# Performance work log

Hardware: AMD Instinct MI355X
Metric: run time of the kernel (lower is better)

The kernel has to match this reference:

```python
import jax, jax.numpy as jnp
import numpy as np

EPS = 1e-12  # torch F.normalize default eps


def setup_inputs() -> dict:
    key = jax.random.key(0)
    ks = jax.random.split(key, 7)
    dim, heads = 128, 8
    b, c, s, h, w = 2, dim, 3, 128, 128
    sc = 1.0 / np.sqrt(dim)
    return {
        "x": jax.random.normal(ks[0], (b, c, s, h, w), dtype=jnp.float32),
        "Wq": jax.random.normal(ks[1], (dim, dim), dtype=jnp.float32) * sc,
        "Wk": jax.random.normal(ks[2], (dim, dim), dtype=jnp.float32) * sc,
        "Wv": jax.random.normal(ks[3], (dim, dim), dtype=jnp.float32) * sc,
        "Wp": jax.random.normal(ks[4], (dim, dim), dtype=jnp.float32) * sc,
        "bp": jax.random.normal(ks[5], (dim,), dtype=jnp.float32) * 0.01,
        "rescale": jnp.ones((heads, 1, 1), dtype=jnp.float32),
    }


def _l2norm(t):
    # torch F.normalize(p=2, dim=-1): t / max(||t||, eps)
    n = jnp.sqrt(jnp.sum(t * t, axis=-1, keepdims=True))
    return t / jnp.maximum(n, EPS)


def reference(x, Wq, Wk, Wv, Wp, bp, rescale):
    b, c, s, h, w = x.shape
    heads = rescale.shape[0]
    d = c // heads
    n = h * w * s
    # [b,c,s,h,w] -> [b,h,w,s,c] -> [b, n, c]
    xt = jnp.transpose(x, (0, 3, 4, 2, 1)).reshape(b, n, c)
    # torch Linear: y = x @ W.T
    q = xt @ Wq.T
    k = xt @ Wk.T
    v = xt @ Wv.T
    # [b,n,heads,d] -> [b,heads,d,n] (channel attention: tokens along last axis)
    def to_heads(t):
        return jnp.transpose(t.reshape(b, n, heads, d), (0, 2, 3, 1))
    q, k, v = to_heads(q), to_heads(k), to_heads(v)
    q = _l2norm(q)
    k = _l2norm(k)
    # attn: [b,heads,d,d] = k @ q^T over token axis n
    attn = jnp.einsum('bhdn,bhen->bhde', k, q)
    attn = attn * rescale  # rescale broadcasts as [heads,1,1]
    attn = jax.nn.softmax(attn, axis=-1)
    out = jnp.einsum('bhde,bhen->bhdn', attn, v)  # [b,heads,d,n]
    # [b,heads,d,n] -> [b,n,heads*d]
    out = jnp.transpose(out, (0, 3, 1, 2)).reshape(b, n, c)
    out = out @ Wp.T + bp
    # [b,n,c] -> [b,h,w,s,c] -> [b,h,w,c,s] -> [b,c,s,h,w]
    out = out.reshape(b, h, w, s, c)
    out = jnp.transpose(out, (0, 1, 2, 4, 3))
    out = jnp.transpose(out, (0, 3, 4, 1, 2))
    return out
```

## Files before the change

kernel.cpp:

```cpp
#include <hip/hip_runtime.h>
#include <hip/hip_bf16.h>

typedef __bf16 bf16_t;
typedef __bf16 bf16x4 __attribute__((ext_vector_type(4)));
typedef __bf16 bf16x8 __attribute__((ext_vector_type(8)));
typedef float f32x4 __attribute__((ext_vector_type(4)));

#define NTOK 49152
#define CDIM 128
#define CHUNKS 128
#define KT 384
#define STEPS 12

__device__ inline f32x4 mfma16(bf16x8 a, bf16x8 b, f32x4 c) {
  return __builtin_amdgcn_mfma_f32_16x16x32_bf16(a, b, c, 0, 0, 0);
}

#define BARRIER() do { asm volatile("s_waitcnt lgkmcnt(0)" ::: "memory"); \
    __builtin_amdgcn_s_barrier(); } while (0)

__global__ __launch_bounds__(256) void k1_gram(const float* __restrict__ x,
                                               float* __restrict__ part) {
  const int blk = blockIdx.x;
  const int b = blk >> 7, chunk = blk & 127;
  const float* Xb = x + (size_t)b * CDIM * NTOK;
  const int tid = threadIdx.x, wave = tid >> 6, lane = tid & 63;

  __shared__ __align__(16) bf16_t tile[2][128 * 32];

  const int sch = tid >> 1, shalf = tid & 1;
  const float* gsrc = Xb + (size_t)sch * NTOK + chunk * KT + shalf * 16;
  const int c16base = ((sch >> 4) << 6) + (sch & 15);
  const int cg0 = c16base + ((shalf * 2) << 4);
  const int cg1 = c16base + ((shalf * 2 + 1) << 4);

  f32x4 stA[4], stB[4];
#define STAGE_LOAD(st, step)                               \
  {                                                        \
    const float* p_ = gsrc + (step) * 32;                  \
    st[0] = *(const f32x4*)(p_ + 0);                       \
    st[1] = *(const f32x4*)(p_ + 4);                       \
    st[2] = *(const f32x4*)(p_ + 8);                       \
    st[3] = *(const f32x4*)(p_ + 12);                      \
  }
#define CVT4(v) (bf16x4){(bf16_t)(v)[0], (bf16_t)(v)[1], (bf16_t)(v)[2], (bf16_t)(v)[3]}
#define STAGE_WRITE(st, buf)                               \
  {                                                        \
    bf16_t* t_ = &tile[buf][0];                            \
    *(bf16x4*)&t_[cg0 * 8 + 0] = CVT4(st[0]);              \
    *(bf16x4*)&t_[cg0 * 8 + 4] = CVT4(st[1]);              \
    *(bf16x4*)&t_[cg1 * 8 + 0] = CVT4(st[2]);              \
    *(bf16x4*)&t_[cg1 * 8 + 4] = CVT4(st[3]);              \
  }

  f32x4 acc[2][8];
#pragma unroll
  for (int t = 0; t < 2; ++t)
#pragma unroll
    for (int j = 0; j < 8; ++j) acc[t][j] = (f32x4){0.f, 0.f, 0.f, 0.f};

#define MFMA_PHASE(buf)                                                     \
  {                                                                         \
    bf16x8 frag[8];                                                         \
    _Pragma("unroll")                                                       \
    for (int g = 0; g < 8; ++g)                                             \
      frag[g] = *(const bf16x8*)&tile[buf][(g * 64 + lane) * 8];            \
    bf16x8 a0, a1;                                                          \
    if (wave == 0)      { a0 = frag[0]; a1 = frag[1]; }                     \
    else if (wave == 1) { a0 = frag[2]; a1 = frag[3]; }                     \
    else if (wave == 2) { a0 = frag[4]; a1 = frag[5]; }                     \
    else                { a0 = frag[6]; a1 = frag[7]; }                     \
    _Pragma("unroll")                                                       \
    for (int j = 0; j < 8; ++j) {                                           \
      acc[0][j] = mfma16(a0, frag[j], acc[0][j]);                           \
      acc[1][j] = mfma16(a1, frag[j], acc[1][j]);                           \
    }                                                                       \
  }

  STAGE_LOAD(stA, 0);
  STAGE_WRITE(stA, 0);
  STAGE_LOAD(stB, 1);
  BARRIER();

  for (int kk = 0; kk < STEPS; kk += 2) {
    if (kk + 2 < STEPS) STAGE_LOAD(stA, kk + 2);
    STAGE_WRITE(stB, 1);
    MFMA_PHASE(0);
    BARRIER();
    if (kk + 3 < STEPS) STAGE_LOAD(stB, kk + 3);
    if (kk + 2 < STEPS) STAGE_WRITE(stA, 0);
    MFMA_PHASE(1);
    BARRIER();
  }
#undef STAGE_LOAD
#undef STAGE_WRITE
#undef MFMA_PHASE

  float* pb = part + ((size_t)(b * CHUNKS + chunk) << 14);
#pragma unroll
  for (int t = 0; t < 2; ++t)
#pragma unroll
    for (int j = 0; j < 8; ++j)
      *(f32x4*)&pb[((((t * 8 + j) << 8) + tid) << 2)] = acc[t][j];
}

__global__ __launch_bounds__(256) void k2a_reduce(const float* __restrict__ part,
                                                  float* __restrict__ part2) {
  const int gid = blockIdx.x * 256 + threadIdx.x;
  const int e4 = gid & 4095, sl = (gid >> 12) & 7, b = gid >> 15;
  const float* p = part + ((size_t)(b * CHUNKS + sl * 16) << 14) + e4 * 4;
  f32x4 s = (f32x4){0.f, 0.f, 0.f, 0.f};
#pragma unroll 8
  for (int i = 0; i < 16; ++i) s += *(const f32x4*)(p + ((size_t)i << 14));
  *(f32x4*)(part2 + ((size_t)(b * 8 + sl) << 14) + e4 * 4) = s;
}

__global__ __launch_bounds__(256) void k2b_reduce(const float* __restrict__ part2,
                                                  float* __restrict__ S) {
  const int gid = blockIdx.x * 256 + threadIdx.x;
  const int g4 = gid & 4095, b = gid >> 12;
  f32x4 s = (f32x4){0.f, 0.f, 0.f, 0.f};
#pragma unroll
  for (int sl = 0; sl < 8; ++sl)
    s += *(const f32x4*)(part2 + ((size_t)(b * 8 + sl) << 14) + g4 * 4);
  const int tj = g4 >> 8, t = tj >> 3, j = tj & 7;
  const int tid2 = g4 & 255, wave = tid2 >> 6, quad = (tid2 >> 4) & 3, r = tid2 & 15;
  const int row0 = wave * 32 + t * 16 + quad * 4, col = j * 16 + r;
  float* Sb = S + ((size_t)b << 14);
#pragma unroll
  for (int reg = 0; reg < 4; ++reg) Sb[(row0 + reg) * 128 + col] = s[reg];
}

__global__ __launch_bounds__(256) void k3_t(const float* __restrict__ S,
                                            const float* __restrict__ Wk,
                                            const float* __restrict__ Wq,
                                            float* __restrict__ Tm) {
  const int idx = blockIdx.x * 256 + threadIdx.x;
  const int j = idx & 127, i = (idx >> 7) & 127, t = (idx >> 14) & 1, b = idx >> 15;
  const f32x4* w4 = (const f32x4*)((t ? Wq : Wk) + i * 128);
  const f32x4* s4 = (const f32x4*)(S + (b << 14) + j * 128);
  float s = 0.f;
#pragma unroll 8
  for (int q = 0; q < 32; ++q) {
    const f32x4 a = w4[q], v = s4[q];
    s += a[0] * v[0] + a[1] * v[1] + a[2] * v[2] + a[3] * v[3];
  }
  Tm[idx] = s;
}

__global__ __launch_bounds__(256) void k3_attn(const float* __restrict__ Tm,
                                               const float* __restrict__ Wk,
                                               const float* __restrict__ Wq,
                                               const float* __restrict__ resc,
                                               float* __restrict__ attn) {
  const int blk = blockIdx.x;
  const int b = blk >> 3, h = blk & 7;
  const int tid = threadIdx.x, d = tid >> 4, e = tid & 15;
  const float* Tk = Tm + (size_t)(b * 2 + 0) * 16384;
  const float* Tq = Tm + (size_t)(b * 2 + 1) * 16384;

  const float* tkrow = Tk + (h * 16 + d) * 128;
  const float* wqrow = Wq + (h * 16 + e) * 128;
  float g = 0.f;
#pragma unroll 4
  for (int c = 0; c < 128; ++c) g += tkrow[c] * wqrow[c];

  __shared__ float sqk[16], sqq[16];
  if (e == 0) {
    const float* wkrow = Wk + (h * 16 + d) * 128;
    float s = 0.f;
    for (int c = 0; c < 128; ++c) s += tkrow[c] * wkrow[c];
    sqk[d] = s;
  }
  if (d == 0) {
    const float* tqrow = Tq + (h * 16 + e) * 128;
    float s = 0.f;
    for (int c = 0; c < 128; ++c) s += tqrow[c] * wqrow[c];
    sqq[e] = s;
  }
  __syncthreads();

  const float nk = fmaxf(sqrtf(fmaxf(sqk[d], 0.f)), 1e-12f);
  const float nq = fmaxf(sqrtf(fmaxf(sqq[e], 0.f)), 1e-12f);
  float pre = g / (nk * nq) * resc[h];

  float mx = pre;
#pragma unroll
  for (int m = 1; m < 16; m <<= 1) mx = fmaxf(mx, __shfl_xor(mx, m, 64));
  const float p = expf(pre - mx);
  float sum = p;
#pragma unroll
  for (int m = 1; m < 16; m <<= 1) sum += __shfl_xor(sum, m, 64);
  attn[blk * 256 + tid] = p / sum;
}

__global__ __launch_bounds__(256) void k3_p(const float* __restrict__ attn,
                                            const float* __restrict__ Wp,
                                            const float* __restrict__ Wv,
                                            bf16_t* __restrict__ Phi) {
  const int blk = blockIdx.x;
  const int b = blk >> 7, rrow = blk & 127;
  const int tid = threadIdx.x;
  __shared__ float M[128];
  if (tid < 128) {
    const int h = tid >> 4, e = tid & 15;
    const float* A = attn + (size_t)(b * 8 + h) * 256;
    const float* wp = Wp + rrow * 128 + h * 16;
    float m = 0.f;
#pragma unroll
    for (int d = 0; d < 16; ++d) m += wp[d] * A[d * 16 + e];
    M[tid] = m;
  }
  __syncthreads();
  if (tid < 128) {
    const int c = tid;
    float p = 0.f;
#pragma unroll 4
    for (int j = 0; j < 128; ++j) p += M[j] * Wv[j * 128 + c];
    Phi[((size_t)b << 14) + rrow * 128 + c] = (bf16_t)p;
  }
}

__global__ __launch_bounds__(256) void k4_out(const float* __restrict__ x,
                                              const bf16_t* __restrict__ Phi,
                                              const float* __restrict__ bp,
                                              float* __restrict__ out) {
  const int blk = blockIdx.x;
  const int b = blk / 768, tg = blk % 768;
  const float* Xb = x + (size_t)b * CDIM * NTOK;
  const bf16_t* Ph = Phi + ((size_t)b << 14);
  float* Ob = out + (size_t)b * CDIM * NTOK;
  const int tid = threadIdx.x, wave = tid >> 6, lane = tid & 63;
  const int r = lane & 15, quad = lane >> 4;
  const int tok0 = tg * 64;

  __shared__ __align__(16) char smem[64 * 68 * 4];
  bf16_t* tile = (bf16_t*)smem;
  float* tbuf = (float*)smem;

  {
    const int sch = tid >> 1, shalf = tid & 1;
    const float* p = Xb + (size_t)sch * NTOK + tok0 + shalf * 32;
    f32x4 st[8];
#pragma unroll
    for (int q = 0; q < 8; ++q) st[q] = *(const f32x4*)(p + q * 4);
    const int chunk_hi = ((sch >> 5) << 8) + (((sch >> 3) & 3) << 4);
    const int ei = sch & 7;
#pragma unroll
    for (int j = 0; j < 32; ++j) {
      const int tok = shalf * 32 + j;
      const int chunk = chunk_hi + ((tok >> 4) << 6) + (tok & 15);
      tile[chunk * 8 + ei] = (bf16_t)st[j >> 2][j & 3];
    }
  }
  __syncthreads();

  f32x4 acc[8];
#pragma unroll
  for (int m = 0; m < 8; ++m) acc[m] = (f32x4){0.f, 0.f, 0.f, 0.f};

#pragma unroll
  for (int step = 0; step < 4; ++step) {
    const bf16x8 bfr = *(const bf16x8*)&tile[(step * 256 + wave * 64 + lane) * 8];
#pragma unroll
    for (int m = 0; m < 8; ++m) {
      const bf16x8 ah = *(const bf16x8*)(Ph + (16 * m + r) * 128 + step * 32 + quad * 8);
      acc[m] = mfma16(ah, bfr, acc[m]);
    }
  }

  __syncthreads();
#pragma unroll
  for (int half = 0; half < 2; ++half) {
#pragma unroll
    for (int mm = 0; mm < 4; ++mm) {
#pragma unroll
      for (int reg = 0; reg < 4; ++reg)
        tbuf[(mm * 16 + quad * 4 + reg) * 68 + wave * 16 + r] = acc[half * 4 + mm][reg];
    }
    __syncthreads();
#pragma unroll
    for (int rep = 0; rep < 4; ++rep) {
      const int idx = rep * 256 + tid, rloc = idx >> 4, g = idx & 15;
      f32x4 v = *(const f32x4*)&tbuf[rloc * 68 + g * 4];
      const int row = half * 64 + rloc;
      const float bb = bp[row];
      v[0] += bb; v[1] += bb; v[2] += bb; v[3] += bb;
      *(f32x4*)&Ob[(size_t)row * NTOK + tok0 + g * 4] = v;
    }
    if (half == 0) __syncthreads();
  }
}

extern "C" void kernel_launch(void* const* d_in, const int* in_sizes, int n_in,
                              void* d_out, int out_size, void* d_ws, size_t ws_size,
                              hipStream_t stream) {
  const float* x    = (const float*)d_in[0];
  const float* Wq   = (const float*)d_in[1];
  const float* Wk   = (const float*)d_in[2];
  const float* Wv   = (const float*)d_in[3];
  const float* Wp   = (const float*)d_in[4];
  const float* bp   = (const float*)d_in[5];
  const float* resc = (const float*)d_in[6];
  float* out = (float*)d_out;

  char* ws = (char*)d_ws;
  float*  S    = (float*)(ws + 0);
  float*  Tm   = (float*)(ws + 131072);
  float*  attn = (float*)(ws + 393216);
  bf16_t* Phi  = (bf16_t*)(ws + 409600);
  float* part  = (float*)d_out;
  float* part2 = (float*)((char*)d_out + 16777216);

  k1_gram<<<2 * CHUNKS, 256, 0, stream>>>(x, part);
  k2a_reduce<<<256, 256, 0, stream>>>(part, part2);
  k2b_reduce<<<32, 256, 0, stream>>>(part2, S);
  k3_t<<<256, 256, 0, stream>>>(S, Wk, Wq, Tm);
  k3_attn<<<16, 256, 0, stream>>>(Tm, Wk, Wq, resc, attn);
  k3_p<<<256, 256, 0, stream>>>(attn, Wp, Wv, Phi);
  k4_out<<<1536, 256, 0, stream>>>(x, Phi, bp, out);
}
```

Baseline: 180.0 us.

## Fuse all seven stages into one cooperative kernel with grid syncs

```diff
diff --git a/kernel.cpp b/kernel.cpp
--- a/kernel.cpp
+++ b/kernel.cpp
@@ -1,5 +1,8 @@
 #include <hip/hip_runtime.h>
 #include <hip/hip_bf16.h>
+#include <hip/hip_cooperative_groups.h>
+
+namespace cg = cooperative_groups;
 
 typedef __bf16 bf16_t;
 typedef __bf16 bf16x4 __attribute__((ext_vector_type(4)));
@@ -19,22 +22,6 @@
 #define BARRIER() do { asm volatile("s_waitcnt lgkmcnt(0)" ::: "memory"); \
     __builtin_amdgcn_s_barrier(); } while (0)
 
-__global__ __launch_bounds__(256) void k1_gram(const float* __restrict__ x,
-                                               float* __restrict__ part) {
-  const int blk = blockIdx.x;
-  const int b = blk >> 7, chunk = blk & 127;
-  const float* Xb = x + (size_t)b * CDIM * NTOK;
-  const int tid = threadIdx.x, wave = tid >> 6, lane = tid & 63;
-
-  __shared__ __align__(16) bf16_t tile[2][128 * 32];
-
-  const int sch = tid >> 1, shalf = tid & 1;
-  const float* gsrc = Xb + (size_t)sch * NTOK + chunk * KT + shalf * 16;
-  const int c16base = ((sch >> 4) << 6) + (sch & 15);
-  const int cg0 = c16base + ((shalf * 2) << 4);
-  const int cg1 = c16base + ((shalf * 2 + 1) << 4);
-
-  f32x4 stA[4], stB[4];
 #define STAGE_LOAD(st, step)                               \
   {                                                        \
     const float* p_ = gsrc + (step) * 32;                  \
@@ -52,13 +39,6 @@
     *(bf16x4*)&t_[cg1 * 8 + 0] = CVT4(st[2]);              \
     *(bf16x4*)&t_[cg1 * 8 + 4] = CVT4(st[3]);              \
   }
-
-  f32x4 acc[2][8];
-#pragma unroll
-  for (int t = 0; t < 2; ++t)
-#pragma unroll
-    for (int j = 0; j < 8; ++j) acc[t][j] = (f32x4){0.f, 0.f, 0.f, 0.f};
-
 #define MFMA_PHASE(buf)                                                     \
   {                                                                         \
     bf16x8 frag[8];                                                         \
@@ -77,6 +57,259 @@
     }                                                                       \
   }
 
+__global__ __launch_bounds__(256) void fused_all(
+    const float* x, const float* Wq, const float* Wk, const float* Wv,
+    const float* Wp, const float* bp, const float* resc,
+    float* S, float* Tm, float* attn, bf16_t* Phi, float* out) {
+  cg::grid_group grid = cg::this_grid();
+  const int blk = blockIdx.x;
+  const int tid = threadIdx.x, wave = tid >> 6, lane = tid & 63;
+  const int r = lane & 15, quad = lane >> 4;
+  float* part  = out;
+  float* part2 = out + (16777216 / 4);
+
+  __shared__ __align__(16) char smem[64 * 68 * 4];
+
+  {
+    bf16_t (*tile)[128 * 32] = (bf16_t (*)[128 * 32])smem;
+    const int b = blk >> 7, chunk = blk & 127;
+    const float* Xb = x + (size_t)b * CDIM * NTOK;
+    const int sch = tid >> 1, shalf = tid & 1;
+    const float* gsrc = Xb + (size_t)sch * NTOK + chunk * KT + shalf * 16;
+    const int c16base = ((sch >> 4) << 6) + (sch & 15);
+    const int cg0 = c16base + ((shalf * 2) << 4);
+    const int cg1 = c16base + ((shalf * 2 + 1) << 4);
+
+    f32x4 stA[4], stB[4];
+    f32x4 acc[2][8];
+#pragma unroll
+    for (int t = 0; t < 2; ++t)
+#pragma unroll
+      for (int j = 0; j < 8; ++j) acc[t][j] = (f32x4){0.f, 0.f, 0.f, 0.f};
+
+    STAGE_LOAD(stA, 0);
+    STAGE_WRITE(stA, 0);
+    STAGE_LOAD(stB, 1);
+    BARRIER();
+
+    for (int kk = 0; kk < STEPS; kk += 2) {
+      if (kk + 2 < STEPS) STAGE_LOAD(stA, kk + 2);
+      STAGE_WRITE(stB, 1);
+      MFMA_PHASE(0);
+      BARRIER();
+      if (kk + 3 < STEPS) STAGE_LOAD(stB, kk + 3);
+      if (kk + 2 < STEPS) STAGE_WRITE(stA, 0);
+      MFMA_PHASE(1);
+      BARRIER();
+    }
+
+    float* pb = part + ((size_t)(b * CHUNKS + chunk) << 14);
+#pragma unroll
+    for (int t = 0; t < 2; ++t)
+#pragma unroll
+      for (int j = 0; j < 8; ++j)
+        *(f32x4*)&pb[((((t * 8 + j) << 8) + tid) << 2)] = acc[t][j];
+  }
+  grid.sync();
+
+  {
+    const int gid = blk * 256 + tid;
+    const int e4 = gid & 4095, sl = (gid >> 12) & 7, b = gid >> 15;
+    const float* p = part + ((size_t)(b * CHUNKS + sl * 16) << 14) + e4 * 4;
+    f32x4 s0 = (f32x4){0.f, 0.f, 0.f, 0.f}, s1 = (f32x4){0.f, 0.f, 0.f, 0.f};
+#pragma unroll 4
+    for (int i = 0; i < 16; i += 2) {
+      s0 += *(const f32x4*)(p + ((size_t)i << 14));
+      s1 += *(const f32x4*)(p + ((size_t)(i + 1) << 14));
+    }
+    f32x4 s = s0 + s1;
+    *(f32x4*)(part2 + ((size_t)(b * 8 + sl) << 14) + e4 * 4) = s;
+  }
+  grid.sync();
+
+  if (blk < 32) {
+    const int gid = blk * 256 + tid;
+    const int g4 = gid & 4095, b = gid >> 12;
+    f32x4 s = (f32x4){0.f, 0.f, 0.f, 0.f};
+#pragma unroll
+    for (int sl = 0; sl < 8; ++sl)
+      s += *(const f32x4*)(part2 + ((size_t)(b * 8 + sl) << 14) + g4 * 4);
+    const int tj = g4 >> 8, t = tj >> 3, j = tj & 7;
+    const int tid2 = g4 & 255, w2 = tid2 >> 6, q2 = (tid2 >> 4) & 3, r2 = tid2 & 15;
+    const int row0 = w2 * 32 + t * 16 + q2 * 4, col = j * 16 + r2;
+    float* Sb = S + ((size_t)b << 14);
+#pragma unroll
+    for (int reg = 0; reg < 4; ++reg) Sb[(row0 + reg) * 128 + col] = s[reg];
+  }
+  grid.sync();
+
+  {
+    const int idx = blk * 256 + tid;
+    const int j = idx & 127, i = (idx >> 7) & 127, t = (idx >> 14) & 1, b = idx >> 15;
+    const f32x4* w4 = (const f32x4*)((t ? Wq : Wk) + i * 128);
+    const f32x4* s4 = (const f32x4*)(S + (b << 14) + j * 128);
+    float s = 0.f;
+#pragma unroll 8
+    for (int q = 0; q < 32; ++q) {
+      const f32x4 a = w4[q], v = s4[q];
+      s += a[0] * v[0] + a[1] * v[1] + a[2] * v[2] + a[3] * v[3];
+    }
+    Tm[idx] = s;
+  }
+  grid.sync();
+
+  if (blk < 16) {
+    const int b = blk >> 3, h = blk & 7;
+    const int d = tid >> 4, e = tid & 15;
+    const float* Tk = Tm + (size_t)(b * 2 + 0) * 16384;
+    const float* Tq = Tm + (size_t)(b * 2 + 1) * 16384;
+    const float* tkrow = Tk + (h * 16 + d) * 128;
+    const float* wqrow = Wq + (h * 16 + e) * 128;
+    float g = 0.f;
+#pragma unroll 4
+    for (int c = 0; c < 128; ++c) g += tkrow[c] * wqrow[c];
+
+    float* sqk = (float*)smem;
+    float* sqq = sqk + 16;
+    if (e == 0) {
+      const float* wkrow = Wk + (h * 16 + d) * 128;
+      float s = 0.f;
+      for (int c = 0; c < 128; ++c) s += tkrow[c] * wkrow[c];
+      sqk[d] = s;
+    }
+    if (d == 0) {
+      const float* tqrow = Tq + (h * 16 + e) * 128;
+      float s = 0.f;
+      for (int c = 0; c < 128; ++c) s += tqrow[c] * wqrow[c];
+      sqq[e] = s;
+    }
+    __syncthreads();
+
+    const float nk = fmaxf(sqrtf(fmaxf(sqk[d], 0.f)), 1e-12f);
+    const float nq = fmaxf(sqrtf(fmaxf(sqq[e], 0.f)), 1e-12f);
+    float pre = g / (nk * nq) * resc[h];
+    float mx = pre;
+#pragma unroll
+    for (int m = 1; m < 16; m <<= 1) mx = fmaxf(mx, __shfl_xor(mx, m, 64));
+    const float p = expf(pre - mx);
+    float sum = p;
+#pragma unroll
+    for (int m = 1; m < 16; m <<= 1) sum += __shfl_xor(sum, m, 64);
+    attn[blk * 256 + tid] = p / sum;
+  }
+  grid.sync();
+
+  {
+    const int b = blk >> 7, rrow = blk & 127;
+    float* M = (float*)smem;
+    if (tid < 128) {
+      const int h = tid >> 4, e = tid & 15;
+      const float* A = attn + (size_t)(b * 8 + h) * 256;
+      const float* wp = Wp + rrow * 128 + h * 16;
+      float m = 0.f;
+#pragma unroll
+      for (int dd = 0; dd < 16; ++dd) m += wp[dd] * A[dd * 16 + e];
+      M[tid] = m;
+    }
+    __syncthreads();
+    if (tid < 128) {
+      const int c = tid;
+      float p = 0.f;
+#pragma unroll 4
+      for (int j = 0; j < 128; ++j) p += M[j] * Wv[j * 128 + c];
+      Phi[((size_t)b << 14) + rrow * 128 + c] = (bf16_t)p;
+    }
+  }
+  grid.sync();
+
+#pragma unroll 1
+  for (int it = 0; it < 6; ++it) {
+    __syncthreads();
+    const int tgi = it * 256 + blk;
+    const int b = tgi / 768, tg = tgi % 768;
+    const float* Xb = x + (size_t)b * CDIM * NTOK;
+    const bf16_t* Ph = Phi + ((size_t)b << 14);
+    float* Ob = out + (size_t)b * CDIM * NTOK;
+    const int tok0 = tg * 64;
+    bf16_t* tile4 = (bf16_t*)smem;
+    float* tbuf = (float*)smem;
+
+    {
+      const int sch = tid >> 1, shalf = tid & 1;
+      const float* p = Xb + (size_t)sch * NTOK + tok0 + shalf * 32;
+      f32x4 st[8];
+#pragma unroll
+      for (int q = 0; q < 8; ++q) st[q] = *(const f32x4*)(p + q * 4);
+      const int chunk_hi = ((sch >> 5) << 8) + (((sch >> 3) & 3) << 4);
+      const int ei = sch & 7;
+#pragma unroll
+      for (int j = 0; j < 32; ++j) {
+        const int tok = shalf * 32 + j;
+        const int chunk = chunk_hi + ((tok >> 4) << 6) + (tok & 15);
+        tile4[chunk * 8 + ei] = (bf16_t)st[j >> 2][j & 3];
+      }
+    }
+    __syncthreads();
+
+    f32x4 acc4[8];
+#pragma unroll
+    for (int m = 0; m < 8; ++m) acc4[m] = (f32x4){0.f, 0.f, 0.f, 0.f};
+#pragma unroll
+    for (int step = 0; step < 4; ++step) {
+      const bf16x8 bfr = *(const bf16x8*)&tile4[(step * 256 + wave * 64 + lane) * 8];
+#pragma unroll
+      for (int m = 0; m < 8; ++m) {
+        const bf16x8 ah = *(const bf16x8*)(Ph + (16 * m + r) * 128 + step * 32 + quad * 8);
+        acc4[m] = mfma16(ah, bfr, acc4[m]);
+      }
+    }
+    __syncthreads();
+
+#pragma unroll
+    for (int half = 0; half < 2; ++half) {
+#pragma unroll
+      for (int mm = 0; mm < 4; ++mm) {
+#pragma unroll
+        for (int reg = 0; reg < 4; ++reg)
+          tbuf[(mm * 16 + quad * 4 + reg) * 68 + wave * 16 + r] = acc4[half * 4 + mm][reg];
+      }
+      __syncthreads();
+#pragma unroll
+      for (int rep = 0; rep < 4; ++rep) {
+        const int idx = rep * 256 + tid, rloc = idx >> 4, gg = idx & 15;
+        f32x4 v = *(const f32x4*)&tbuf[rloc * 68 + gg * 4];
+        const int row = half * 64 + rloc;
+        const float bb = bp[row];
+        v[0] += bb; v[1] += bb; v[2] += bb; v[3] += bb;
+        *(f32x4*)&Ob[(size_t)row * NTOK + tok0 + gg * 4] = v;
+      }
+      if (half == 0) __syncthreads();
+    }
+  }
+}
+
+__global__ __launch_bounds__(256) void k1_gram(const float* __restrict__ x,
+                                               float* __restrict__ part) {
+  const int blk = blockIdx.x;
+  const int b = blk >> 7, chunk = blk & 127;
+  const float* Xb = x + (size_t)b * CDIM * NTOK;
+  const int tid = threadIdx.x, wave = tid >> 6, lane = tid & 63;
+
+  __shared__ __align__(16) bf16_t tile[2][128 * 32];
+
+  const int sch = tid >> 1, shalf = tid & 1;
+  const float* gsrc = Xb + (size_t)sch * NTOK + chunk * KT + shalf * 16;
+  const int c16base = ((sch >> 4) << 6) + (sch & 15);
+  const int cg0 = c16base + ((shalf * 2) << 4);
+  const int cg1 = c16base + ((shalf * 2 + 1) << 4);
+
+  f32x4 stA[4], stB[4];
+  f32x4 acc[2][8];
+#pragma unroll
+  for (int t = 0; t < 2; ++t)
+#pragma unroll
+    for (int j = 0; j < 8; ++j) acc[t][j] = (f32x4){0.f, 0.f, 0.f, 0.f};
+
   STAGE_LOAD(stA, 0);
   STAGE_WRITE(stA, 0);
   STAGE_LOAD(stB, 1);
@@ -92,9 +325,6 @@
     MFMA_PHASE(1);
     BARRIER();
   }
-#undef STAGE_LOAD
-#undef STAGE_WRITE
-#undef MFMA_PHASE
 
   float* pb = part + ((size_t)(b * CHUNKS + chunk) << 14);
 #pragma unroll
@@ -312,11 +542,21 @@
   float* part  = (float*)d_out;
   float* part2 = (float*)((char*)d_out + 16777216);
 
-  k1_gram<<<2 * CHUNKS, 256, 0, stream>>>(x, part);
-  k2a_reduce<<<256, 256, 0, stream>>>(part, part2);
-  k2b_reduce<<<32, 256, 0, stream>>>(part2, S);
-  k3_t<<<256, 256, 0, stream>>>(S, Wk, Wq, Tm);
-  k3_attn<<<16, 256, 0, stream>>>(Tm, Wk, Wq, resc, attn);
-  k3_p<<<256, 256, 0, stream>>>(attn, Wp, Wv, Phi);
-  k4_out<<<1536, 256, 0, stream>>>(x, Phi, bp, out);
-}
+  const float *a0 = x, *a1 = Wq, *a2 = Wk, *a3 = Wv, *a4 = Wp, *a5 = bp, *a6 = resc;
+  float *a7 = S, *a8 = Tm, *a9 = attn;
+  bf16_t* a10 = Phi;
+  float* a11 = out;
+  void* args[12] = {&a0, &a1, &a2, &a3, &a4, &a5, &a6, &a7, &a8, &a9, &a10, &a11};
+  hipError_t err = hipLaunchCooperativeKernel((const void*)fused_all, dim3(256),
+                                              dim3(256), args, 0, stream);
+  if (err != hipSuccess) {
+    (void)hipGetLastError();
+    k1_gram<<<2 * CHUNKS, 256, 0, stream>>>(x, part);
+    k2a_reduce<<<256, 256, 0, stream>>>(part, part2);
+    k2b_reduce<<<32, 256, 0, stream>>>(part2, S);
+    k3_t<<<256, 256, 0, stream>>>(S, Wk, Wq, Tm);
+    k3_attn<<<16, 256, 0, stream>>>(Tm, Wk, Wq, resc, attn);
+    k3_p<<<256, 256, 0, stream>>>(attn, Wp, Wv, Phi);
+    k4_out<<<1536, 256, 0, stream>>>(x, Phi, bp, out);
+  }
+}
```

New measurement: 369.6 us. +105.4%, slower.

## Fuse gram reduction into k1 and collapse middle kernels into one grid-synced kernel

Applied to the files above, without the earlier changes.

```diff
diff --git a/kernel.cpp b/kernel.cpp
--- a/kernel.cpp
+++ b/kernel.cpp
@@ -19,22 +19,6 @@
 #define BARRIER() do { asm volatile("s_waitcnt lgkmcnt(0)" ::: "memory"); \
     __builtin_amdgcn_s_barrier(); } while (0)
 
-__global__ __launch_bounds__(256) void k1_gram(const float* __restrict__ x,
-                                               float* __restrict__ part) {
-  const int blk = blockIdx.x;
-  const int b = blk >> 7, chunk = blk & 127;
-  const float* Xb = x + (size_t)b * CDIM * NTOK;
-  const int tid = threadIdx.x, wave = tid >> 6, lane = tid & 63;
-
-  __shared__ __align__(16) bf16_t tile[2][128 * 32];
-
-  const int sch = tid >> 1, shalf = tid & 1;
-  const float* gsrc = Xb + (size_t)sch * NTOK + chunk * KT + shalf * 16;
-  const int c16base = ((sch >> 4) << 6) + (sch & 15);
-  const int cg0 = c16base + ((shalf * 2) << 4);
-  const int cg1 = c16base + ((shalf * 2 + 1) << 4);
-
-  f32x4 stA[4], stB[4];
 #define STAGE_LOAD(st, step)                               \
   {                                                        \
     const float* p_ = gsrc + (step) * 32;                  \
@@ -52,13 +36,6 @@
     *(bf16x4*)&t_[cg1 * 8 + 0] = CVT4(st[2]);              \
     *(bf16x4*)&t_[cg1 * 8 + 4] = CVT4(st[3]);              \
   }
-
-  f32x4 acc[2][8];
-#pragma unroll
-  for (int t = 0; t < 2; ++t)
-#pragma unroll
-    for (int j = 0; j < 8; ++j) acc[t][j] = (f32x4){0.f, 0.f, 0.f, 0.f};
-
 #define MFMA_PHASE(buf)                                                     \
   {                                                                         \
     bf16x8 frag[8];                                                         \
@@ -77,6 +54,30 @@
     }                                                                       \
   }
 
+__global__ __launch_bounds__(256) void k1_gramred(const float* __restrict__ x,
+                                                  float* __restrict__ part,
+                                                  float* __restrict__ part2,
+                                                  int* __restrict__ cnt) {
+  const int blk = blockIdx.x;
+  const int b = blk >> 7, chunk = blk & 127;
+  const float* Xb = x + (size_t)b * CDIM * NTOK;
+  const int tid = threadIdx.x, wave = tid >> 6, lane = tid & 63;
+
+  __shared__ __align__(16) bf16_t tile[2][128 * 32];
+
+  const int sch = tid >> 1, shalf = tid & 1;
+  const float* gsrc = Xb + (size_t)sch * NTOK + chunk * KT + shalf * 16;
+  const int c16base = ((sch >> 4) << 6) + (sch & 15);
+  const int cg0 = c16base + ((shalf * 2) << 4);
+  const int cg1 = c16base + ((shalf * 2 + 1) << 4);
+
+  f32x4 stA[4], stB[4];
+  f32x4 acc[2][8];
+#pragma unroll
+  for (int t = 0; t < 2; ++t)
+#pragma unroll
+    for (int j = 0; j < 8; ++j) acc[t][j] = (f32x4){0.f, 0.f, 0.f, 0.f};
+
   STAGE_LOAD(stA, 0);
   STAGE_WRITE(stA, 0);
   STAGE_LOAD(stB, 1);
@@ -92,9 +93,6 @@
     MFMA_PHASE(1);
     BARRIER();
   }
-#undef STAGE_LOAD
-#undef STAGE_WRITE
-#undef MFMA_PHASE
 
   float* pb = part + ((size_t)(b * CHUNKS + chunk) << 14);
 #pragma unroll
@@ -102,122 +100,186 @@
 #pragma unroll
     for (int j = 0; j < 8; ++j)
       *(f32x4*)&pb[((((t * 8 + j) << 8) + tid) << 2)] = acc[t][j];
-}
-
-__global__ __launch_bounds__(256) void k2a_reduce(const float* __restrict__ part,
-                                                  float* __restrict__ part2) {
-  const int gid = blockIdx.x * 256 + threadIdx.x;
-  const int e4 = gid & 4095, sl = (gid >> 12) & 7, b = gid >> 15;
-  const float* p = part + ((size_t)(b * CHUNKS + sl * 16) << 14) + e4 * 4;
-  f32x4 s = (f32x4){0.f, 0.f, 0.f, 0.f};
-#pragma unroll 8
-  for (int i = 0; i < 16; ++i) s += *(const f32x4*)(p + ((size_t)i << 14));
-  *(f32x4*)(part2 + ((size_t)(b * 8 + sl) << 14) + e4 * 4) = s;
-}
-
-__global__ __launch_bounds__(256) void k2b_reduce(const float* __restrict__ part2,
-                                                  float* __restrict__ S) {
-  const int gid = blockIdx.x * 256 + threadIdx.x;
-  const int g4 = gid & 4095, b = gid >> 12;
-  f32x4 s = (f32x4){0.f, 0.f, 0.f, 0.f};
-#pragma unroll
-  for (int sl = 0; sl < 8; ++sl)
-    s += *(const f32x4*)(part2 + ((size_t)(b * 8 + sl) << 14) + g4 * 4);
-  const int tj = g4 >> 8, t = tj >> 3, j = tj & 7;
-  const int tid2 = g4 & 255, wave = tid2 >> 6, quad = (tid2 >> 4) & 3, r = tid2 & 15;
-  const int row0 = wave * 32 + t * 16 + quad * 4, col = j * 16 + r;
-  float* Sb = S + ((size_t)b << 14);
-#pragma unroll
-  for (int reg = 0; reg < 4; ++reg) Sb[(row0 + reg) * 128 + col] = s[reg];
-}
-
-__global__ __launch_bounds__(256) void k3_t(const float* __restrict__ S,
+
+  __threadfence();
+  __syncthreads();
+  __shared__ int lastf;
+  if (tid == 0)
+    lastf = (atomicAdd(&cnt[b * 8 + (chunk >> 4)], 1) == 15) ? 1 : 0;
+  __syncthreads();
+  if (lastf) {
+    __threadfence();
+    const int g = chunk >> 4;
+    const float* src0 = part + ((size_t)(b * CHUNKS + g * 16) << 14);
+    float* dst = part2 + ((size_t)(b * 8 + g) << 14);
+#pragma unroll 1
+    for (int k = 0; k < 16; ++k) {
+      const int idx4 = k * 256 + tid;
+      f32x4 s = (f32x4){0.f, 0.f, 0.f, 0.f};
+#pragma unroll
+      for (int i = 0; i < 16; ++i)
+        s += *(const f32x4*)(src0 + (((size_t)i) << 14) + idx4 * 4);
+      *(f32x4*)(dst + idx4 * 4) = s;
+    }
+  }
+}
+
+__global__ __launch_bounds__(256) void kmid(const float* __restrict__ part2,
                                             const float* __restrict__ Wk,
                                             const float* __restrict__ Wq,
-                                            float* __restrict__ Tm) {
-  const int idx = blockIdx.x * 256 + threadIdx.x;
-  const int j = idx & 127, i = (idx >> 7) & 127, t = (idx >> 14) & 1, b = idx >> 15;
-  const f32x4* w4 = (const f32x4*)((t ? Wq : Wk) + i * 128);
-  const f32x4* s4 = (const f32x4*)(S + (b << 14) + j * 128);
-  float s = 0.f;
-#pragma unroll 8
-  for (int q = 0; q < 32; ++q) {
-    const f32x4 a = w4[q], v = s4[q];
-    s += a[0] * v[0] + a[1] * v[1] + a[2] * v[2] + a[3] * v[3];
-  }
-  Tm[idx] = s;
-}
-
-__global__ __launch_bounds__(256) void k3_attn(const float* __restrict__ Tm,
-                                               const float* __restrict__ Wk,
-                                               const float* __restrict__ Wq,
-                                               const float* __restrict__ resc,
-                                               float* __restrict__ attn) {
+                                            const float* __restrict__ Wp,
+                                            const float* __restrict__ Wv,
+                                            const float* __restrict__ resc,
+                                            float* __restrict__ Mbuf,
+                                            bf16_t* __restrict__ Phi,
+                                            int* __restrict__ cntM) {
   const int blk = blockIdx.x;
   const int b = blk >> 3, h = blk & 7;
-  const int tid = threadIdx.x, d = tid >> 4, e = tid & 15;
-  const float* Tk = Tm + (size_t)(b * 2 + 0) * 16384;
-  const float* Tq = Tm + (size_t)(b * 2 + 1) * 16384;
-
-  const float* tkrow = Tk + (h * 16 + d) * 128;
-  const float* wqrow = Wq + (h * 16 + e) * 128;
-  float g = 0.f;
-#pragma unroll 4
-  for (int c = 0; c < 128; ++c) g += tkrow[c] * wqrow[c];
-
-  __shared__ float sqk[16], sqq[16];
-  if (e == 0) {
-    const float* wkrow = Wk + (h * 16 + d) * 128;
-    float s = 0.f;
-    for (int c = 0; c < 128; ++c) s += tkrow[c] * wkrow[c];
-    sqk[d] = s;
-  }
-  if (d == 0) {
-    const float* tqrow = Tq + (h * 16 + e) * 128;
-    float s = 0.f;
-    for (int c = 0; c < 128; ++c) s += tqrow[c] * wqrow[c];
-    sqq[e] = s;
-  }
-  __syncthreads();
-
-  const float nk = fmaxf(sqrtf(fmaxf(sqk[d], 0.f)), 1e-12f);
-  const float nq = fmaxf(sqrtf(fmaxf(sqq[e], 0.f)), 1e-12f);
-  float pre = g / (nk * nq) * resc[h];
-
-  float mx = pre;
-#pragma unroll
-  for (int m = 1; m < 16; m <<= 1) mx = fmaxf(mx, __shfl_xor(mx, m, 64));
-  const float p = expf(pre - mx);
-  float sum = p;
-#pragma unroll
-  for (int m = 1; m < 16; m <<= 1) sum += __shfl_xor(sum, m, 64);
-  attn[blk * 256 + tid] = p / sum;
-}
-
-__global__ __launch_bounds__(256) void k3_p(const float* __restrict__ attn,
-                                            const float* __restrict__ Wp,
-                                            const float* __restrict__ Wv,
-                                            bf16_t* __restrict__ Phi) {
-  const int blk = blockIdx.x;
-  const int b = blk >> 7, rrow = blk & 127;
   const int tid = threadIdx.x;
-  __shared__ float M[128];
-  if (tid < 128) {
-    const int h = tid >> 4, e = tid & 15;
-    const float* A = attn + (size_t)(b * 8 + h) * 256;
-    const float* wp = Wp + rrow * 128 + h * 16;
-    float m = 0.f;
-#pragma unroll
-    for (int d = 0; d < 16; ++d) m += wp[d] * A[d * 16 + e];
-    M[tid] = m;
-  }
-  __syncthreads();
-  if (tid < 128) {
-    const int c = tid;
-    float p = 0.f;
-#pragma unroll 4
-    for (int j = 0; j < 128; ++j) p += M[j] * Wv[j * 128 + c];
-    Phi[((size_t)b << 14) + rrow * 128 + c] = (bf16_t)p;
+
+  __shared__ float S_l[128][132];
+  __shared__ float Wk_l[16][128], Wq_l[16][128];
+  __shared__ float Tk_l[16][132], Tq_l[16][132];
+  __shared__ float A_l[16][16];
+  __shared__ float dK[16], dQ[16];
+
+  {
+    const float* p0 = part2 + ((size_t)(b * 8) << 14);
+#pragma unroll 1
+    for (int k = 0; k < 16; ++k) {
+      const int g4 = k * 256 + tid;
+      f32x4 s = (f32x4){0.f, 0.f, 0.f, 0.f};
+#pragma unroll
+      for (int sl = 0; sl < 8; ++sl)
+        s += *(const f32x4*)(p0 + ((size_t)sl << 14) + g4 * 4);
+      const int tj = g4 >> 8, t_ = tj >> 3, j_ = tj & 7;
+      const int t2 = g4 & 255, w2 = t2 >> 6, q2 = (t2 >> 4) & 3, r2 = t2 & 15;
+      const int row0 = w2 * 32 + t_ * 16 + q2 * 4, col = j_ * 16 + r2;
+#pragma unroll
+      for (int reg = 0; reg < 4; ++reg) S_l[row0 + reg][col] = s[reg];
+    }
+#pragma unroll
+    for (int k = 0; k < 8; ++k) {
+      const int idx = k * 256 + tid;
+      Wk_l[idx >> 7][idx & 127] = Wk[h * 2048 + idx];
+      Wq_l[idx >> 7][idx & 127] = Wq[h * 2048 + idx];
+    }
+  }
+  __syncthreads();
+
+  {
+    const int d2 = tid >> 5;
+    const int j0 = (tid & 31) * 4;
+    f32x4 aK0 = (f32x4){0.f,0.f,0.f,0.f}, aK1 = (f32x4){0.f,0.f,0.f,0.f};
+    f32x4 aQ0 = (f32x4){0.f,0.f,0.f,0.f}, aQ1 = (f32x4){0.f,0.f,0.f,0.f};
+#pragma unroll 1
+    for (int cb = 0; cb < 4; ++cb) {
+      f32x4 wk0[8], wk1[8], wq0[8], wq1[8];
+#pragma unroll
+      for (int q = 0; q < 8; ++q) {
+        wk0[q] = *(const f32x4*)&Wk_l[d2][cb * 32 + q * 4];
+        wk1[q] = *(const f32x4*)&Wk_l[d2 + 8][cb * 32 + q * 4];
+        wq0[q] = *(const f32x4*)&Wq_l[d2][cb * 32 + q * 4];
+        wq1[q] = *(const f32x4*)&Wq_l[d2 + 8][cb * 32 + q * 4];
+      }
+#pragma unroll
+      for (int q = 0; q < 8; ++q) {
+#pragma unroll
+        for (int cc = 0; cc < 4; ++cc) {
+          const int c = cb * 32 + q * 4 + cc;
+          const f32x4 sv = *(const f32x4*)&S_l[c][j0];
+          aK0 += sv * wk0[q][cc];
+          aK1 += sv * wk1[q][cc];
+          aQ0 += sv * wq0[q][cc];
+          aQ1 += sv * wq1[q][cc];
+        }
+      }
+    }
+    *(f32x4*)&Tk_l[d2][j0]     = aK0;
+    *(f32x4*)&Tk_l[d2 + 8][j0] = aK1;
+    *(f32x4*)&Tq_l[d2][j0]     = aQ0;
+    *(f32x4*)&Tq_l[d2 + 8][j0] = aQ1;
+  }
+  __syncthreads();
+
+  {
+    const int d = tid >> 4, e = tid & 15;
+    f32x4 gacc = (f32x4){0.f,0.f,0.f,0.f};
+    f32x4 kacc = (f32x4){0.f,0.f,0.f,0.f};
+    f32x4 qacc = (f32x4){0.f,0.f,0.f,0.f};
+#pragma unroll
+    for (int j4 = 0; j4 < 32; ++j4) {
+      const f32x4 tk = *(const f32x4*)&Tk_l[d][j4 * 4];
+      const f32x4 wq = *(const f32x4*)&Wq_l[e][j4 * 4];
+      gacc += tk * wq;
+      if (e == 0) kacc += tk * (*(const f32x4*)&Wk_l[d][j4 * 4]);
+      if (d == 0) qacc += (*(const f32x4*)&Tq_l[e][j4 * 4]) * wq;
+    }
+    if (e == 0) dK[d] = kacc[0] + kacc[1] + kacc[2] + kacc[3];
+    if (d == 0) dQ[e] = qacc[0] + qacc[1] + qacc[2] + qacc[3];
+    __syncthreads();
+    const float g = gacc[0] + gacc[1] + gacc[2] + gacc[3];
+    const float nk = fmaxf(sqrtf(fmaxf(dK[d], 0.f)), 1e-12f);
+    const float nq = fmaxf(sqrtf(fmaxf(dQ[e], 0.f)), 1e-12f);
+    float pre = g / (nk * nq) * resc[h];
+    float mx = pre;
+#pragma unroll
+    for (int m = 1; m < 16; m <<= 1) mx = fmaxf(mx, __shfl_xor(mx, m, 64));
+    const float p = expf(pre - mx);
+    float sum = p;
+#pragma unroll
+    for (int m = 1; m < 16; m <<= 1) sum += __shfl_xor(sum, m, 64);
+    A_l[d][e] = p / sum;
+  }
+  __syncthreads();
+
+  {
+    const int e = tid & 15, rg = tid >> 4;
+#pragma unroll
+    for (int k = 0; k < 8; ++k) {
+      const int r = rg * 8 + k;
+      const f32x4* wp4 = (const f32x4*)(Wp + r * 128 + h * 16);
+      float m = 0.f;
+#pragma unroll
+      for (int q = 0; q < 4; ++q) {
+        const f32x4 w = wp4[q];
+        m += w[0] * A_l[q * 4 + 0][e] + w[1] * A_l[q * 4 + 1][e] +
+             w[2] * A_l[q * 4 + 2][e] + w[3] * A_l[q * 4 + 3][e];
+      }
+      Mbuf[(size_t)b * 16384 + r * 128 + h * 16 + e] = m;
+    }
+  }
+
+  __threadfence();
+  __syncthreads();
+  if (tid == 0) {
+    atomicAdd(&cntM[b], 1);
+    while (__hip_atomic_load(&cntM[b], __ATOMIC_RELAXED,
+                             __HIP_MEMORY_SCOPE_AGENT) < 8)
+      __builtin_amdgcn_s_sleep(16);
+  }
+  __syncthreads();
+  __threadfence();
+
+  {
+    const int cc = tid & 15, rg = tid >> 4;
+    const float* Mb = Mbuf + (size_t)b * 16384;
+    float pacc[8] = {0.f, 0.f, 0.f, 0.f, 0.f, 0.f, 0.f, 0.f};
+#pragma unroll 2
+    for (int j4 = 0; j4 < 32; ++j4) {
+      float wv[4];
+#pragma unroll
+      for (int jj = 0; jj < 4; ++jj)
+        wv[jj] = Wv[(j4 * 4 + jj) * 128 + h * 16 + cc];
+#pragma unroll
+      for (int k = 0; k < 8; ++k) {
+        const f32x4 m4 = *(const f32x4*)&Mb[(rg * 8 + k) * 128 + j4 * 4];
+        pacc[k] += m4[0] * wv[0] + m4[1] * wv[1] + m4[2] * wv[2] + m4[3] * wv[3];
+      }
+    }
+#pragma unroll
+    for (int k = 0; k < 8; ++k)
+      Phi[((size_t)b << 14) + (rg * 8 + k) * 128 + h * 16 + cc] = (bf16_t)pacc[k];
   }
 }
 
@@ -305,18 +367,15 @@
   float* out = (float*)d_out;
 
   char* ws = (char*)d_ws;
-  float*  S    = (float*)(ws + 0);
-  float*  Tm   = (float*)(ws + 131072);
-  float*  attn = (float*)(ws + 393216);
-  bf16_t* Phi  = (bf16_t*)(ws + 409600);
+  float*  Mbuf = (float*)(ws + 0);
+  bf16_t* Phi  = (bf16_t*)(ws + 131072);
+  int*    cnt  = (int*)(ws + 196608);
+  int*    cntM = cnt + 16;
   float* part  = (float*)d_out;
   float* part2 = (float*)((char*)d_out + 16777216);
 
-  k1_gram<<<2 * CHUNKS, 256, 0, stream>>>(x, part);
-  k2a_reduce<<<256, 256, 0, stream>>>(part, part2);
-  k2b_reduce<<<32, 256, 0, stream>>>(part2, S);
-  k3_t<<<256, 256, 0, stream>>>(S, Wk, Wq, Tm);
-  k3_attn<<<16, 256, 0, stream>>>(Tm, Wk, Wq, resc, attn);
-  k3_p<<<256, 256, 0, stream>>>(attn, Wp, Wv, Phi);
+  (void)hipMemsetAsync(ws + 196608, 0, 128, stream);
+  k1_gramred<<<2 * CHUNKS, 256, 0, stream>>>(x, part, part2, cnt);
+  kmid<<<16, 256, 0, stream>>>(part2, Wk, Wq, Wp, Wv, resc, Mbuf, Phi, cntM);
   k4_out<<<1536, 256, 0, stream>>>(x, Phi, bp, out);
 }
```

New measurement: 226.9 us. +26.1%, slower.
